# Optimization experiments

Measured on AMD Instinct MI355X. Metric: run time of the kernel, lower is better.

Reference implementation:

```python
import jax, jax.numpy as jnp
import numpy as np

N = 50000
E = 800000
IN, H, OUT = 128, 96, 64
BN_EPS = 1e-5


def setup_inputs() -> dict:
    key = jax.random.key(0)
    ks = jax.random.split(key, 16)
    x = jax.random.normal(ks[0], (N, IN), dtype=jnp.float32)
    edge_index = jax.random.randint(ks[1], (2, E), 0, N, dtype=jnp.int64)
    edge_weight = jax.random.uniform(ks[2], (E,), dtype=jnp.float32)
    def lin(k, fo, fi):
        # PyG glorot-ish init
        s = 1.0 / np.sqrt(fi)
        return jax.random.uniform(k, (fo, fi), minval=-s, maxval=s, dtype=jnp.float32)
    W1, b1 = lin(ks[3], H, IN), jnp.zeros((H,), jnp.float32)
    W2, b2 = lin(ks[4], H, H), jnp.zeros((H,), jnp.float32)
    W3, b3 = lin(ks[5], OUT, H), jnp.zeros((OUT,), jnp.float32)
    g1 = jnp.ones((H,), jnp.float32); beta1 = jnp.zeros((H,), jnp.float32)
    m1 = 0.1 * jax.random.normal(ks[6], (H,), dtype=jnp.float32)
    v1 = jnp.abs(1.0 + 0.1 * jax.random.normal(ks[7], (H,), dtype=jnp.float32))
    g2 = jnp.ones((H,), jnp.float32); beta2 = jnp.zeros((H,), jnp.float32)
    m2 = 0.1 * jax.random.normal(ks[8], (H,), dtype=jnp.float32)
    v2 = jnp.abs(1.0 + 0.1 * jax.random.normal(ks[9], (H,), dtype=jnp.float32))
    return dict(x=x, edge_index=edge_index, edge_weight=edge_weight,
                W1=W1, b1=b1, W2=W2, b2=b2, W3=W3, b3=b3,
                g1=g1, beta1=beta1, m1=m1, v1=v1,
                g2=g2, beta2=beta2, m2=m2, v2=v2)


def gcn_norm(edge_index, edge_weight, n):
    # PyG gcn_norm with add_self_loops=True, fill_value=1.0
    loop = jnp.arange(n, dtype=edge_index.dtype)
    row = jnp.concatenate([edge_index[0], loop])  # sources
    col = jnp.concatenate([edge_index[1], loop])  # targets
    ew = jnp.concatenate([edge_weight, jnp.ones((n,), edge_weight.dtype)])
    deg = jax.ops.segment_sum(ew, col, num_segments=n)
    dis = jnp.where(deg > 0, jax.lax.rsqrt(deg), 0.0)  # inf -> 0 masked_fill
    norm = dis[row] * ew * dis[col]
    return row, col, norm


def gcn_conv(x, row, col, norm, W, b, n):
    xw = x @ W.T                       # [N, F_out] dense transform first
    msg = norm[:, None] * xw[row]      # [E+N, F_out] gather + edge scale
    out = jax.ops.segment_sum(msg, col, num_segments=n)  # scatter-add
    return out + b


def bn_eval(x, gamma, beta, mean, var):
    return (x - mean) * jax.lax.rsqrt(var + BN_EPS) * gamma + beta


def reference(x, edge_index, edge_weight, W1, b1, W2, b2, W3, b3,
              g1, beta1, m1, v1, g2, beta2, m2, v2):
    n = x.shape[0]
    row, col, norm = gcn_norm(edge_index, edge_weight, n)  # cached=True: shared
    h = gcn_conv(x, row, col, norm, W1, b1, n)
    h = jax.nn.relu(bn_eval(h, g1, beta1, m1, v1))
    h = gcn_conv(h, row, col, norm, W2, b2, n)
    h = jax.nn.relu(bn_eval(h, g2, beta2, m2, v2))
    out = gcn_conv(h, row, col, norm, W3, b3, n)
    return out
```

## Files before the change

### kernel.cpp

```cpp
#include <hip/hip_runtime.h>
#include <hip/hip_fp16.h>


constexpr float BN_EPS = 1e-5f;
constexpr float DEG_SCALE = 131072.0f;
constexpr float INV_DEG_SCALE = 1.0f / 131072.0f;
constexpr float NORM_SCALE = 32768.0f;
constexpr float INV_NORM_SCALE = 1.0f / 32768.0f;

typedef _Float16 f16x8 __attribute__((ext_vector_type(8)));
typedef float f32x4 __attribute__((ext_vector_type(4)));


__device__ __forceinline__ void gemm1_q(const float* __restrict__ x,
                                        const float* __restrict__ W1,
                                        unsigned char* __restrict__ t1q,
                                        float* __restrict__ scl1,
                                        int n0b, int tid, int n,
                                        _Float16* lds, unsigned* rmaxb) {
    constexpr int LROW = 104;
    if (tid < 64) rmaxb[tid] = 0u;
    int wave = tid >> 6, lane = tid & 63, quad = lane >> 4, r = lane & 15;
    int n0 = n0b + wave * 16;
    if (n0 < n) {
        f16x8 a[4];
        const float* xr = x + (size_t)(n0 + r) * 128 + quad * 8;
#pragma unroll
        for (int kt = 0; kt < 4; ++kt) {
            float4 v0 = *(const float4*)(xr + kt * 32);
            float4 v1 = *(const float4*)(xr + kt * 32 + 4);
            f16x8 t = {(_Float16)v0.x, (_Float16)v0.y, (_Float16)v0.z, (_Float16)v0.w,
                       (_Float16)v1.x, (_Float16)v1.y, (_Float16)v1.z, (_Float16)v1.w};
            a[kt] = t;
        }
        f32x4 acc[6];
#pragma unroll
        for (int ft = 0; ft < 6; ++ft) acc[ft] = (f32x4){0.f, 0.f, 0.f, 0.f};
#pragma unroll
        for (int kt = 0; kt < 4; ++kt) {
#pragma unroll
            for (int ft = 0; ft < 6; ++ft) {
                const float* wr = W1 + (size_t)(ft * 16 + r) * 128 + kt * 32 + quad * 8;
                float4 v0 = *(const float4*)wr;
                float4 v1 = *(const float4*)(wr + 4);
                f16x8 b = {(_Float16)v0.x, (_Float16)v0.y, (_Float16)v0.z, (_Float16)v0.w,
                           (_Float16)v1.x, (_Float16)v1.y, (_Float16)v1.z, (_Float16)v1.w};
                acc[ft] = __builtin_amdgcn_mfma_f32_16x16x32_f16(a[kt], b, acc[ft], 0, 0, 0);
            }
        }
#pragma unroll
        for (int ft = 0; ft < 6; ++ft)
#pragma unroll
            for (int reg = 0; reg < 4; ++reg)
                lds[(size_t)(wave * 16 + quad * 4 + reg) * LROW + ft * 16 + r] =
                    (_Float16)acc[ft][reg];
    }
    __syncthreads();
    {
        int row = tid >> 2, qt = tid & 3;
        const _Float16* lp = lds + (size_t)row * LROW + qt * 24;
        float mx = 0.f;
#pragma unroll
        for (int j = 0; j < 24; ++j) mx = fmaxf(mx, fabsf((float)lp[j]));
        atomicMax(&rmaxb[row], __float_as_uint(mx));
    }
    __syncthreads();
    for (int i = tid; i < 64 * 12; i += 256) {
        int row = i / 12, c = i - row * 12;
        int grow = n0b + row;
        if (grow >= n) continue;
        float rm = __uint_as_float(rmaxb[row]);
        float inv = (rm > 0.f) ? 127.0f / rm : 0.f;
        const _Float16* lp = lds + (size_t)row * LROW + c * 8;
        unsigned lo = 0, hi = 0;
#pragma unroll
        for (int j = 0; j < 4; ++j) {
            int qv = __float2int_rn((float)lp[j] * inv);
            qv = qv > 127 ? 127 : (qv < -127 ? -127 : qv);
            lo |= ((unsigned)qv & 255u) << (8 * j);
        }
#pragma unroll
        for (int j = 0; j < 4; ++j) {
            int qv = __float2int_rn((float)lp[4 + j] * inv);
            qv = qv > 127 ? 127 : (qv < -127 ? -127 : qv);
            hi |= ((unsigned)qv & 255u) << (8 * j);
        }
        *(uint2*)(t1q + (size_t)grow * 96 + c * 8) = make_uint2(lo, hi);
        if (c == 0) scl1[grow] = rm * (1.0f / 127.0f);
    }
}

__global__ __launch_bounds__(256) void k_mega(
    const int* __restrict__ row_idx, const int* __restrict__ col_idx,
    const float* __restrict__ ew,
    unsigned long long* packed, unsigned char* rank, int e_cnt, int pair_b,
    int t1, int t2,
    const float* __restrict__ x, const float* __restrict__ W1,
    unsigned char* __restrict__ t1q, float* __restrict__ scl1, int n,
    const float* __restrict__ W2, const float* __restrict__ W3,
    _Float16* __restrict__ w2h, _Float16* __restrict__ w3h,
    int w2n4, int w3n4) {
    __shared__ _Float16 lds[64 * 104];
    __shared__ unsigned rmaxb[64];
    int b = blockIdx.x;
    if (b < 2 * pair_b) {
        int q = b >> 1;
        if ((b & 1) == 0) {
#pragma unroll
            for (int j = 0; j < 4; ++j) {
                int e = q * 1024 + j * 256 + (int)threadIdx.x;
                if (e < e_cnt) {
                    int c = col_idx[e];
                    int r = row_idx[e];
                    int t = (r >= t2) ? 2 : ((r >= t1) ? 1 : 0);
                    int sh = 24 + 10 * t;
                    unsigned wfix = (unsigned)(ew[e] * DEG_SCALE + 0.5f);
                    unsigned long long inc = (1ull << sh) | (unsigned long long)wfix;
                    unsigned long long old = atomicAdd(&packed[c], inc);
                    rank[e] = (unsigned char)((old >> sh) & 0x3FFull);
                }
            }
        } else {
            gemm1_q(x, W1, t1q, scl1, q * 64, (int)threadIdx.x, n, lds, rmaxb);
        }
    } else {
        int i = (b - 2 * pair_b) * 256 + (int)threadIdx.x;
        const float* src; _Float16* dst; int o;
        if (i < w2n4) { src = W2; dst = w2h; o = i; }
        else if (i < w2n4 + w3n4) { src = W3; dst = w3h; o = i - w2n4; }
        else return;
        float4 v = ((const float4*)src)[o];
        __half2 h0 = __floats2half2_rn(v.x, v.y);
        __half2 h1 = __floats2half2_rn(v.z, v.w);
        *(uint2*)(dst + (size_t)o * 4) = make_uint2(*(unsigned*)&h0, *(unsigned*)&h1);
    }
}


__device__ __forceinline__ int pk_cnt(unsigned long long p) {
    return (int)((p >> 24) & 0x3FF) + (int)((p >> 34) & 0x3FF) + (int)((p >> 44) & 0x3FF);
}

__global__ void k_scan1(const unsigned long long* __restrict__ packed,
                        int* bsum, float* dis, int n) {
    __shared__ int s[256];
    int i = blockIdx.x * 256 + threadIdx.x;
    int cnt = 0;
    if (i < n) {
        unsigned long long p = packed[i];
        cnt = pk_cnt(p);
        float wsum = (float)(unsigned)(p & 0xFFFFFFull) * INV_DEG_SCALE;
        dis[i] = rsqrtf(1.0f + wsum);
    }
    s[threadIdx.x] = cnt;
    __syncthreads();
    for (int off = 128; off > 0; off >>= 1) {
        if ((int)threadIdx.x < off) s[threadIdx.x] += s[threadIdx.x + off];
        __syncthreads();
    }
    if (threadIdx.x == 0) bsum[blockIdx.x] = s[0];
}

__global__ void k_scan23(const unsigned long long* __restrict__ packed,
                         const int* __restrict__ bsum,
                         int* row_ptr, int n, int e_total, int nb) {
    __shared__ int sb[256];
    __shared__ int s[256];
    int t = threadIdx.x;
    int bv = (t < nb) ? bsum[t] : 0;
    sb[t] = bv;
    __syncthreads();
    for (int off = 1; off < 256; off <<= 1) {
        int x = (t >= off) ? sb[t - off] : 0;
        __syncthreads();
        sb[t] += x;
        __syncthreads();
    }
    int boff = (blockIdx.x == 0) ? 0 : sb[blockIdx.x - 1];

    int i = blockIdx.x * 256 + t;
    int v = (i < n) ? pk_cnt(packed[i]) : 0;
    s[t] = v;
    __syncthreads();
    for (int off = 1; off < 256; off <<= 1) {
        int x = (t >= off) ? s[t - off] : 0;
        __syncthreads();
        s[t] += x;
        __syncthreads();
    }
    int ex = s[t] - v + boff;
    if (i < n) row_ptr[i] = ex;
    if (i == 0) row_ptr[n] = e_total;
}

__global__ void k_fill(const int* __restrict__ row_idx, const int* __restrict__ col_idx,
                       const float* __restrict__ ew, const float* __restrict__ dis,
                       const int* __restrict__ row_ptr, const unsigned char* __restrict__ rank,
                       const unsigned long long* __restrict__ packed,
                       unsigned* ep, int e_cnt, int t1, int t2) {
    int e = blockIdx.x * 256 + threadIdx.x;
    if (e < e_cnt) {
        int r = row_idx[e];
        int c = col_idx[e];
        unsigned long long p = packed[c];
        int c0 = (int)((p >> 24) & 0x3FF);
        int c1 = (int)((p >> 34) & 0x3FF);
        int t = (r >= t2) ? 2 : ((r >= t1) ? 1 : 0);
        int off = (t > 0 ? c0 : 0) + (t > 1 ? c1 : 0);
        float nm = dis[r] * ew[e];
        unsigned q = (unsigned)(nm * NORM_SCALE + 0.5f);
        if (q > 65535u) q = 65535u;
        ep[row_ptr[c] + off + (int)rank[e]] = ((unsigned)r << 16) | q;
    }
}


__device__ inline void cvt8(uint4 u, float* f) {
    float2 t;
    t = __half22float2(*(const __half2*)&u.x); f[0] = t.x; f[1] = t.y;
    t = __half22float2(*(const __half2*)&u.y); f[2] = t.x; f[3] = t.y;
    t = __half22float2(*(const __half2*)&u.z); f[4] = t.x; f[5] = t.y;
    t = __half22float2(*(const __half2*)&u.w); f[6] = t.x; f[7] = t.y;
}

__device__ inline void h8_acc(uint4 u, float w, float acc[8]) {
    float2 a = __half22float2(*(const __half2*)&u.x);
    float2 b = __half22float2(*(const __half2*)&u.y);
    float2 c = __half22float2(*(const __half2*)&u.z);
    float2 d = __half22float2(*(const __half2*)&u.w);
    acc[0] = fmaf(w, a.x, acc[0]); acc[1] = fmaf(w, a.y, acc[1]);
    acc[2] = fmaf(w, b.x, acc[2]); acc[3] = fmaf(w, b.y, acc[3]);
    acc[4] = fmaf(w, c.x, acc[4]); acc[5] = fmaf(w, c.y, acc[5]);
    acc[6] = fmaf(w, d.x, acc[6]); acc[7] = fmaf(w, d.y, acc[7]);
}

__device__ inline void q8_acc(uint2 v, float ws, float acc[8]) {
    int a = (int)v.x, b = (int)v.y;
    acc[0] = fmaf(ws, (float)(int)(char)(a      ), acc[0]);
    acc[1] = fmaf(ws, (float)(int)(char)(a >>  8), acc[1]);
    acc[2] = fmaf(ws, (float)(int)(char)(a >> 16), acc[2]);
    acc[3] = fmaf(ws, (float)(a >> 24),            acc[3]);
    acc[4] = fmaf(ws, (float)(int)(char)(b      ), acc[4]);
    acc[5] = fmaf(ws, (float)(int)(char)(b >>  8), acc[5]);
    acc[6] = fmaf(ws, (float)(int)(char)(b >> 16), acc[6]);
    acc[7] = fmaf(ws, (float)(b >> 24),            acc[7]);
}

__device__ __forceinline__ void gather_row_q(const unsigned char* __restrict__ tq,
                                             const float* __restrict__ scl,
                                             const unsigned* __restrict__ ep,
                                             int e0, int e1, int q, float acc[8]) {
    int e = e0;
    for (; e + 4 <= e1; e += 4) {
        unsigned p0 = ep[e + 0], p1 = ep[e + 1], p2 = ep[e + 2], p3 = ep[e + 3];
        uint2 v0 = *(const uint2*)(tq + (size_t)(p0 >> 16) * 96 + q * 8);
        uint2 v1 = *(const uint2*)(tq + (size_t)(p1 >> 16) * 96 + q * 8);
        uint2 v2 = *(const uint2*)(tq + (size_t)(p2 >> 16) * 96 + q * 8);
        uint2 v3 = *(const uint2*)(tq + (size_t)(p3 >> 16) * 96 + q * 8);
        float s0 = scl[p0 >> 16], s1 = scl[p1 >> 16];
        float s2 = scl[p2 >> 16], s3 = scl[p3 >> 16];
        q8_acc(v0, (float)(p0 & 0xffffu) * INV_NORM_SCALE * s0, acc);
        q8_acc(v1, (float)(p1 & 0xffffu) * INV_NORM_SCALE * s1, acc);
        q8_acc(v2, (float)(p2 & 0xffffu) * INV_NORM_SCALE * s2, acc);
        q8_acc(v3, (float)(p3 & 0xffffu) * INV_NORM_SCALE * s3, acc);
    }
    for (; e < e1; ++e) {
        unsigned p = ep[e];
        uint2 v = *(const uint2*)(tq + (size_t)(p >> 16) * 96 + q * 8);
        q8_acc(v, (float)(p & 0xffffu) * INV_NORM_SCALE * scl[p >> 16], acc);
    }
}

template <int FQ>
__device__ __forceinline__ void gather_row(const uint4* __restrict__ base,
                                           const unsigned* __restrict__ ep,
                                           int e0, int e1, int q, float acc[8]) {
    int e = e0;
    for (; e + 8 <= e1; e += 8) {
        unsigned p0 = ep[e + 0], p1 = ep[e + 1], p2 = ep[e + 2], p3 = ep[e + 3];
        unsigned p4 = ep[e + 4], p5 = ep[e + 5], p6 = ep[e + 6], p7 = ep[e + 7];
        uint4 x0 = base[(size_t)(p0 >> 16) * FQ + q];
        uint4 x1 = base[(size_t)(p1 >> 16) * FQ + q];
        uint4 x2 = base[(size_t)(p2 >> 16) * FQ + q];
        uint4 x3 = base[(size_t)(p3 >> 16) * FQ + q];
        uint4 x4 = base[(size_t)(p4 >> 16) * FQ + q];
        uint4 x5 = base[(size_t)(p5 >> 16) * FQ + q];
        uint4 x6 = base[(size_t)(p6 >> 16) * FQ + q];
        uint4 x7 = base[(size_t)(p7 >> 16) * FQ + q];
        h8_acc(x0, (float)(p0 & 0xffffu) * INV_NORM_SCALE, acc);
        h8_acc(x1, (float)(p1 & 0xffffu) * INV_NORM_SCALE, acc);
        h8_acc(x2, (float)(p2 & 0xffffu) * INV_NORM_SCALE, acc);
        h8_acc(x3, (float)(p3 & 0xffffu) * INV_NORM_SCALE, acc);
        h8_acc(x4, (float)(p4 & 0xffffu) * INV_NORM_SCALE, acc);
        h8_acc(x5, (float)(p5 & 0xffffu) * INV_NORM_SCALE, acc);
        h8_acc(x6, (float)(p6 & 0xffffu) * INV_NORM_SCALE, acc);
        h8_acc(x7, (float)(p7 & 0xffffu) * INV_NORM_SCALE, acc);
    }
    for (; e + 4 <= e1; e += 4) {
        unsigned p0 = ep[e + 0], p1 = ep[e + 1], p2 = ep[e + 2], p3 = ep[e + 3];
        uint4 x0 = base[(size_t)(p0 >> 16) * FQ + q];
        uint4 x1 = base[(size_t)(p1 >> 16) * FQ + q];
        uint4 x2 = base[(size_t)(p2 >> 16) * FQ + q];
        uint4 x3 = base[(size_t)(p3 >> 16) * FQ + q];
        h8_acc(x0, (float)(p0 & 0xffffu) * INV_NORM_SCALE, acc);
        h8_acc(x1, (float)(p1 & 0xffffu) * INV_NORM_SCALE, acc);
        h8_acc(x2, (float)(p2 & 0xffffu) * INV_NORM_SCALE, acc);
        h8_acc(x3, (float)(p3 & 0xffffu) * INV_NORM_SCALE, acc);
    }
    for (; e < e1; ++e) {
        unsigned p = ep[e];
        uint4 xv = base[(size_t)(p >> 16) * FQ + q];
        h8_acc(xv, (float)(p & 0xffffu) * INV_NORM_SCALE, acc);
    }
}


template <int FOUT, bool QOUT>
__global__ __launch_bounds__(192) void k_aggr_mm(
    const unsigned char* __restrict__ tq, const float* __restrict__ scl,
    const int* __restrict__ row_ptr, const unsigned* __restrict__ ep,
    const float* __restrict__ dis, const float* __restrict__ bias,
    const float* __restrict__ g, const float* __restrict__ beta,
    const float* __restrict__ m, const float* __restrict__ v,
    const _Float16* __restrict__ Wh,
    void* __restrict__ Yout, float* __restrict__ sclo, int n) {
    constexpr int LROW = 104;
    __shared__ _Float16 lds[16 * LROW];
    __shared__ unsigned rmaxb[16];
    int tid = (int)threadIdx.x;
    int n0b = blockIdx.x * 16;
    int nl = tid / 12;
    int q = tid - nl * 12;
    int node = n0b + nl;
    if (QOUT && tid < 16) rmaxb[tid] = 0u;

    if (node < n) {
        float d = dis[node];
        float acc[8];
#pragma unroll
        for (int j = 0; j < 8; ++j) acc[j] = 0.f;
        {
            uint2 sv = *(const uint2*)(tq + (size_t)node * 96 + q * 8);
            q8_acc(sv, d * scl[node], acc);
        }
        gather_row_q(tq, scl, ep, row_ptr[node], row_ptr[node + 1], q, acc);

        int fb = q * 8;
        const float4* bb = (const float4*)(bias + fb);
        float4 b0 = bb[0], b1 = bb[1];
        acc[0] = fmaf(acc[0], d, b0.x); acc[1] = fmaf(acc[1], d, b0.y);
        acc[2] = fmaf(acc[2], d, b0.z); acc[3] = fmaf(acc[3], d, b0.w);
        acc[4] = fmaf(acc[4], d, b1.x); acc[5] = fmaf(acc[5], d, b1.y);
        acc[6] = fmaf(acc[6], d, b1.z); acc[7] = fmaf(acc[7], d, b1.w);
#pragma unroll
        for (int j = 0; j < 8; ++j) {
            acc[j] = fmaxf((acc[j] - m[fb + j]) * rsqrtf(v[fb + j] + BN_EPS) * g[fb + j]
                           + beta[fb + j], 0.f);
        }
        __half2 h0 = __floats2half2_rn(acc[0], acc[1]);
        __half2 h1 = __floats2half2_rn(acc[2], acc[3]);
        __half2 h2 = __floats2half2_rn(acc[4], acc[5]);
        __half2 h3 = __floats2half2_rn(acc[6], acc[7]);
        *(uint4*)(lds + (size_t)nl * LROW + fb) =
            make_uint4(*(unsigned*)&h0, *(unsigned*)&h1, *(unsigned*)&h2, *(unsigned*)&h3);
    }
    __syncthreads();

    constexpr int FT = FOUT / 16;
    f32x4 cacc[FT];
    int quad = tid >> 4, r = tid & 15;
    if (tid < 64) {
        f16x8 a[3];
#pragma unroll
        for (int kt = 0; kt < 3; ++kt)
            a[kt] = *(const f16x8*)(lds + (size_t)r * LROW + kt * 32 + quad * 8);
#pragma unroll
        for (int ft = 0; ft < FT; ++ft) cacc[ft] = (f32x4){0.f, 0.f, 0.f, 0.f};
#pragma unroll
        for (int kt = 0; kt < 3; ++kt) {
#pragma unroll
            for (int ft = 0; ft < FT; ++ft) {
                f16x8 b = *(const f16x8*)(Wh + (size_t)(ft * 16 + r) * 96 + kt * 32 + quad * 8);
                cacc[ft] = __builtin_amdgcn_mfma_f32_16x16x32_f16(a[kt], b, cacc[ft], 0, 0, 0);
            }
        }
    }
    __syncthreads();
    if (tid < 64) {
#pragma unroll
        for (int ft = 0; ft < FT; ++ft)
#pragma unroll
            for (int reg = 0; reg < 4; ++reg)
                lds[(size_t)(quad * 4 + reg) * LROW + ft * 16 + r] = (_Float16)cacc[ft][reg];
    }
    __syncthreads();

    if (QOUT) {
        if (tid < 64) {
            int row = tid >> 2, qt = tid & 3;
            const _Float16* lp = lds + (size_t)row * LROW + qt * 24;
            float mx = 0.f;
#pragma unroll
            for (int j = 0; j < 24; ++j) mx = fmaxf(mx, fabsf((float)lp[j]));
            atomicMax(&rmaxb[row], __float_as_uint(mx));
        }
        __syncthreads();
        {
            int row = nl, c = q;
            int grow = n0b + row;
            if (grow < n) {
                float rm = __uint_as_float(rmaxb[row]);
                float inv = (rm > 0.f) ? 127.0f / rm : 0.f;
                const _Float16* lp = lds + (size_t)row * LROW + c * 8;
                unsigned lo = 0, hi = 0;
#pragma unroll
                for (int j = 0; j < 4; ++j) {
                    int qv = __float2int_rn((float)lp[j] * inv);
                    qv = qv > 127 ? 127 : (qv < -127 ? -127 : qv);
                    lo |= ((unsigned)qv & 255u) << (8 * j);
                }
#pragma unroll
                for (int j = 0; j < 4; ++j) {
                    int qv = __float2int_rn((float)lp[4 + j] * inv);
                    qv = qv > 127 ? 127 : (qv < -127 ? -127 : qv);
                    hi |= ((unsigned)qv & 255u) << (8 * j);
                }
                *(uint2*)((unsigned char*)Yout + (size_t)grow * 96 + c * 8) =
                    make_uint2(lo, hi);
                if (c == 0) sclo[grow] = rm * (1.0f / 127.0f);
            }
        }
    } else {
        constexpr int CPR = FOUT / 8;
        for (int i = tid; i < 16 * CPR; i += 192) {
            int row = i / CPR, c = i - row * CPR;
            int grow = n0b + row;
            if (grow < n)
                *(uint4*)((_Float16*)Yout + (size_t)grow * FOUT + c * 8) =
                    *(const uint4*)(lds + (size_t)row * LROW + c * 8);
        }
    }
}


__global__ __launch_bounds__(256) void k_aggr3(
    const _Float16* __restrict__ xw, const int* __restrict__ row_ptr,
    const unsigned* __restrict__ ep,
    const float* __restrict__ dis, const float* __restrict__ bias,
    float* __restrict__ out, int n) {
    constexpr int FQ = 8;
    int tg = blockIdx.x * 256 + threadIdx.x;
    int node = tg / FQ;
    int q = tg - node * FQ;
    if (node >= n) return;

    const uint4* __restrict__ base = (const uint4*)xw;
    float d = dis[node];
    float acc[8];
    {
        uint4 sv = base[(size_t)node * FQ + q];
        float t[8];
        cvt8(sv, t);
#pragma unroll
        for (int j = 0; j < 8; ++j) acc[j] = d * t[j];
    }
    gather_row<FQ>(base, ep, row_ptr[node], row_ptr[node + 1], q, acc);

    int fb = q * 8;
    const float4* bb = (const float4*)(bias + fb);
    float4 b0 = bb[0], b1 = bb[1];
    acc[0] = fmaf(acc[0], d, b0.x); acc[1] = fmaf(acc[1], d, b0.y);
    acc[2] = fmaf(acc[2], d, b0.z); acc[3] = fmaf(acc[3], d, b0.w);
    acc[4] = fmaf(acc[4], d, b1.x); acc[5] = fmaf(acc[5], d, b1.y);
    acc[6] = fmaf(acc[6], d, b1.z); acc[7] = fmaf(acc[7], d, b1.w);

    float* op = out + (size_t)node * 64 + fb;
    *(float4*)(op + 0) = make_float4(acc[0], acc[1], acc[2], acc[3]);
    *(float4*)(op + 4) = make_float4(acc[4], acc[5], acc[6], acc[7]);
}


extern "C" void kernel_launch(void* const* d_in, const int* in_sizes, int n_in,
                              void* d_out, int out_size, void* d_ws, size_t ws_size,
                              hipStream_t stream) {
    constexpr int IN = 128, H = 96, OUT = 64;

    const float* x   = (const float*)d_in[0];
    const int*   ei  = (const int*)d_in[1];
    const float* ew  = (const float*)d_in[2];
    const float* W1  = (const float*)d_in[3];
    const float* b1  = (const float*)d_in[4];
    const float* W2  = (const float*)d_in[5];
    const float* b2  = (const float*)d_in[6];
    const float* W3  = (const float*)d_in[7];
    const float* b3  = (const float*)d_in[8];
    const float* g1  = (const float*)d_in[9];
    const float* be1 = (const float*)d_in[10];
    const float* m1  = (const float*)d_in[11];
    const float* v1  = (const float*)d_in[12];
    const float* g2  = (const float*)d_in[13];
    const float* be2 = (const float*)d_in[14];
    const float* m2  = (const float*)d_in[15];
    const float* v2  = (const float*)d_in[16];

    const int N = in_sizes[0] / IN;
    const int E = in_sizes[2];
    const int* row_idx = ei;
    const int* col_idx = ei + E;
    const int T1 = N / 3, T2 = 2 * (N / 3);

    char* ws = (char*)d_ws;
    size_t off = 0;
    auto alloc = [&](size_t bytes) -> void* {
        void* p = ws + off;
        off = (off + bytes + 255) & ~(size_t)255;
        return p;
    };
    unsigned long long* packed = (unsigned long long*)alloc((size_t)N * 8);
    float*     dis     = (float*)alloc((size_t)N * 4);
    int*       row_ptr = (int*)alloc((size_t)(N + 1) * 4);
    int*       bsum    = (int*)alloc(256 * 4);
    unsigned char* rank = (unsigned char*)alloc((size_t)E);
    unsigned*  ep      = (unsigned*)alloc((size_t)E * 4);
    _Float16*  w2h     = (_Float16*)alloc((size_t)H * H * 2);
    _Float16*  w3h     = (_Float16*)alloc((size_t)OUT * H * 2);
    unsigned char* t1q = (unsigned char*)alloc((size_t)N * 96);
    float*     scl1    = (float*)alloc((size_t)N * 4);
    unsigned char* t2q = (unsigned char*)alloc((size_t)N * 96);
    float*     scl2    = (float*)alloc((size_t)N * 4);
    _Float16*  buf64   = (_Float16*)alloc((size_t)N * OUT * 2);
    (void)ws_size; (void)n_in; (void)out_size;

    constexpr int W2N4 = H * H / 4, W3N4 = OUT * H / 4;
    const int NB = (N + 255) / 256;
    const int DEG1024 = (E + 1023) / 1024;
    const int GG = (N + 63) / 64;
    const int PAIR = (DEG1024 > GG) ? DEG1024 : GG;
    const int CVT_B = (W2N4 + W3N4 + 255) / 256;

    hipMemsetAsync(packed, 0, (size_t)N * 8, stream);
    k_mega<<<2 * PAIR + CVT_B, 256, 0, stream>>>(
        row_idx, col_idx, ew, packed, rank, E, PAIR, T1, T2,
        x, W1, t1q, scl1, N, W2, W3, w2h, w3h, W2N4, W3N4);
    k_scan1<<<NB, 256, 0, stream>>>(packed, bsum, dis, N);
    k_scan23<<<NB, 256, 0, stream>>>(packed, bsum, row_ptr, N, E, NB);
    k_fill<<<(E + 255) / 256, 256, 0, stream>>>(row_idx, col_idx, ew, dis,
                                                row_ptr, rank, packed, ep, E, T1, T2);

    const int GF = (N + 15) / 16;
    const int GA64 = ((size_t)N * (OUT / 8) + 255) / 256;

    k_aggr_mm<H, true><<<GF, 192, 0, stream>>>(
        t1q, scl1, row_ptr, ep, dis, b1, g1, be1, m1, v1, w2h, t2q, scl2, N);

    k_aggr_mm<OUT, false><<<GF, 192, 0, stream>>>(
        t2q, scl2, row_ptr, ep, dis, b2, g2, be2, m2, v2, w3h, buf64, nullptr, N);

    k_aggr3<<<GA64, 256, 0, stream>>>(buf64, row_ptr, ep, dis, b3, (float*)d_out, N);
}
```

Measured before the change: 243.9 us.

## Replace global-atomic CSR build with two-level bucketed counting sort

Builds the destination-sorted edge list with a radix-style two-pass sort instead of per-edge 64-bit global atomics. Each chunk of edges builds a 256-bucket histogram in shared memory, a column scan produces per-chunk bucket bases, and a scatter writes edge records into coarse buckets. A per-bucket fine pass then counts and places edges by destination and source third using shared-memory atomics and computes degrees. A final pass rescales the edge norms by the source degree. This removes global atomic contention and the memset, but adds more kernel launches, an 8-byte intermediate record array, and a serial 768-entry prefix scan done by one thread per block.

```diff
diff --git a/kernel.cpp b/kernel.cpp
--- a/kernel.cpp
+++ b/kernel.cpp
@@ -3,8 +3,6 @@
 
 
 constexpr float BN_EPS = 1e-5f;
-constexpr float DEG_SCALE = 131072.0f;
-constexpr float INV_DEG_SCALE = 1.0f / 131072.0f;
 constexpr float NORM_SCALE = 32768.0f;
 constexpr float INV_NORM_SCALE = 1.0f / 32768.0f;
 
@@ -90,11 +88,12 @@
     }
 }
 
+
 __global__ __launch_bounds__(256) void k_mega(
-    const int* __restrict__ row_idx, const int* __restrict__ col_idx,
-    const float* __restrict__ ew,
-    unsigned long long* packed, unsigned char* rank, int e_cnt, int pair_b,
-    int t1, int t2,
+    const int* __restrict__ col_idx,
+    unsigned* __restrict__ H,
+    unsigned short* __restrict__ lrank,
+    int e_cnt, int pair_b,
     const float* __restrict__ x, const float* __restrict__ W1,
     unsigned char* __restrict__ t1q, float* __restrict__ scl1, int n,
     const float* __restrict__ W2, const float* __restrict__ W3,
@@ -102,24 +101,25 @@
     int w2n4, int w3n4) {
     __shared__ _Float16 lds[64 * 104];
     __shared__ unsigned rmaxb[64];
+    __shared__ unsigned hist[256];
     int b = blockIdx.x;
     if (b < 2 * pair_b) {
         int q = b >> 1;
         if ((b & 1) == 0) {
+            for (int t = threadIdx.x; t < 256; t += 256) hist[t] = 0;
+            __syncthreads();
 #pragma unroll
             for (int j = 0; j < 4; ++j) {
                 int e = q * 1024 + j * 256 + (int)threadIdx.x;
                 if (e < e_cnt) {
-                    int c = col_idx[e];
-                    int r = row_idx[e];
-                    int t = (r >= t2) ? 2 : ((r >= t1) ? 1 : 0);
-                    int sh = 24 + 10 * t;
-                    unsigned wfix = (unsigned)(ew[e] * DEG_SCALE + 0.5f);
-                    unsigned long long inc = (1ull << sh) | (unsigned long long)wfix;
-                    unsigned long long old = atomicAdd(&packed[c], inc);
-                    rank[e] = (unsigned char)((old >> sh) & 0x3FFull);
+                    int bk = col_idx[e] >> 8;
+                    unsigned lr = atomicAdd(&hist[bk], 1u);
+                    lrank[e] = (unsigned short)lr;
                 }
             }
+            __syncthreads();
+            for (int t = threadIdx.x; t < 256; t += 256)
+                H[(size_t)q * 256 + t] = hist[t];
         } else {
             gemm1_q(x, W1, t1q, scl1, q * 64, (int)threadIdx.x, n, lds, rmaxb);
         }
@@ -137,80 +137,137 @@
 }
 
 
-__device__ __forceinline__ int pk_cnt(unsigned long long p) {
-    return (int)((p >> 24) & 0x3FF) + (int)((p >> 34) & 0x3FF) + (int)((p >> 44) & 0x3FF);
-}
-
-__global__ void k_scan1(const unsigned long long* __restrict__ packed,
-                        int* bsum, float* dis, int n) {
-    __shared__ int s[256];
-    int i = blockIdx.x * 256 + threadIdx.x;
-    int cnt = 0;
-    if (i < n) {
-        unsigned long long p = packed[i];
-        cnt = pk_cnt(p);
-        float wsum = (float)(unsigned)(p & 0xFFFFFFull) * INV_DEG_SCALE;
-        dis[i] = rsqrtf(1.0f + wsum);
-    }
-    s[threadIdx.x] = cnt;
-    __syncthreads();
-    for (int off = 128; off > 0; off >>= 1) {
-        if ((int)threadIdx.x < off) s[threadIdx.x] += s[threadIdx.x + off];
+__global__ __launch_bounds__(256) void k_colscan(const unsigned* __restrict__ H,
+                                                 unsigned* __restrict__ Base,
+                                                 unsigned* __restrict__ total,
+                                                 int nblk) {
+    __shared__ unsigned s[256];
+    int bin = blockIdx.x;
+    int t = (int)threadIdx.x;
+    unsigned carry = 0;
+    int nch = (nblk + 255) / 256;
+    for (int c = 0; c < nch; ++c) {
+        int i = c * 256 + t;
+        unsigned v = (i < nblk) ? H[(size_t)i * 256 + bin] : 0;
         __syncthreads();
-    }
-    if (threadIdx.x == 0) bsum[blockIdx.x] = s[0];
-}
-
-__global__ void k_scan23(const unsigned long long* __restrict__ packed,
-                         const int* __restrict__ bsum,
-                         int* row_ptr, int n, int e_total, int nb) {
-    __shared__ int sb[256];
-    __shared__ int s[256];
-    int t = threadIdx.x;
-    int bv = (t < nb) ? bsum[t] : 0;
-    sb[t] = bv;
+        s[t] = v;
+        __syncthreads();
+        for (int off = 1; off < 256; off <<= 1) {
+            unsigned x = (t >= off) ? s[t - off] : 0;
+            __syncthreads();
+            s[t] += x;
+            __syncthreads();
+        }
+        if (i < nblk) Base[(size_t)i * 256 + bin] = carry + s[t] - v;
+        carry += s[255];
+    }
+    if (t == 0) total[bin] = carry;
+}
+
+
+__global__ void k_binoff(const unsigned* __restrict__ total,
+                         unsigned* __restrict__ boff, int nb, int e_total) {
+    __shared__ unsigned s[256];
+    int t = (int)threadIdx.x;
+    unsigned v = (t < nb) ? total[t] : 0;
+    s[t] = v;
     __syncthreads();
     for (int off = 1; off < 256; off <<= 1) {
-        int x = (t >= off) ? sb[t - off] : 0;
-        __syncthreads();
-        sb[t] += x;
-        __syncthreads();
-    }
-    int boff = (blockIdx.x == 0) ? 0 : sb[blockIdx.x - 1];
-
-    int i = blockIdx.x * 256 + t;
-    int v = (i < n) ? pk_cnt(packed[i]) : 0;
-    s[t] = v;
-    __syncthreads();
-    for (int off = 1; off < 256; off <<= 1) {
-        int x = (t >= off) ? s[t - off] : 0;
+        unsigned x = (t >= off) ? s[t - off] : 0;
         __syncthreads();
         s[t] += x;
         __syncthreads();
     }
-    int ex = s[t] - v + boff;
-    if (i < n) row_ptr[i] = ex;
-    if (i == 0) row_ptr[n] = e_total;
-}
-
-__global__ void k_fill(const int* __restrict__ row_idx, const int* __restrict__ col_idx,
-                       const float* __restrict__ ew, const float* __restrict__ dis,
-                       const int* __restrict__ row_ptr, const unsigned char* __restrict__ rank,
-                       const unsigned long long* __restrict__ packed,
-                       unsigned* ep, int e_cnt, int t1, int t2) {
+    if (t < nb) boff[t] = s[t] - v;
+    if (t == 0) boff[nb] = (unsigned)e_total;
+}
+
+
+__global__ __launch_bounds__(256) void k_scatter(
+    const int* __restrict__ row_idx, const int* __restrict__ col_idx,
+    const float* __restrict__ ew, const unsigned short* __restrict__ lrank,
+    const unsigned* __restrict__ Base, const unsigned* __restrict__ boff,
+    unsigned long long* __restrict__ recs, int e_cnt, int nbk) {
+    __shared__ unsigned base[256];
+    int q = blockIdx.x;
+    for (int t = threadIdx.x; t < 256; t += 256)
+        base[t] = (t < nbk) ? (boff[t] + Base[(size_t)q * 256 + t]) : 0u;
+    __syncthreads();
+#pragma unroll
+    for (int j = 0; j < 4; ++j) {
+        int e = q * 1024 + j * 256 + (int)threadIdx.x;
+        if (e < e_cnt) {
+            int c = col_idx[e];
+            int r = row_idx[e];
+            unsigned wfix = (unsigned)(ew[e] * NORM_SCALE + 0.5f);
+            if (wfix > 65535u) wfix = 65535u;
+            unsigned slot = base[c >> 8] + (unsigned)lrank[e];
+            recs[slot] = ((unsigned long long)(unsigned)(c & 255) << 32)
+                       | (unsigned long long)(((unsigned)r << 16) | wfix);
+        }
+    }
+}
+
+
+__global__ __launch_bounds__(256) void k_fine(
+    const unsigned long long* __restrict__ recs, const unsigned* __restrict__ boff,
+    int* __restrict__ row_ptr, float* __restrict__ dis,
+    unsigned* __restrict__ ep, int n, int t1, int t2) {
+    __shared__ unsigned cnt[768];
+    __shared__ unsigned ws[256];
+    int b = blockIdx.x;
+    int tid = (int)threadIdx.x;
+    unsigned e0 = boff[b], e1 = boff[b + 1];
+    for (int i = tid; i < 768; i += 256) cnt[i] = 0;
+    ws[tid] = 0;
+    __syncthreads();
+    for (unsigned e = e0 + (unsigned)tid; e < e1; e += 256) {
+        unsigned long long rec = recs[e];
+        int dlow = (int)((rec >> 32) & 255ull);
+        unsigned lo = (unsigned)rec;
+        int src = (int)(lo >> 16);
+        unsigned wfix = lo & 0xFFFFu;
+        int th = (src >= t2) ? 2 : (src >= t1) ? 1 : 0;
+        atomicAdd(&cnt[dlow * 3 + th], 1u);
+        atomicAdd(&ws[dlow], wfix);
+    }
+    __syncthreads();
+    if (tid == 0) {
+        unsigned run = 0;
+        for (int i = 0; i < 768; ++i) { unsigned v = cnt[i]; cnt[i] = run; run += v; }
+    }
+    __syncthreads();
+    {
+        int dest = b * 256 + tid;
+        if (dest < n) {
+            row_ptr[dest] = (int)(e0 + cnt[tid * 3]);
+            dis[dest] = rsqrtf(1.0f + (float)ws[tid] * INV_NORM_SCALE);
+        }
+        if (b == (int)gridDim.x - 1 && tid == 0) row_ptr[n] = (int)e1;
+    }
+    __syncthreads();
+    for (unsigned e = e0 + (unsigned)tid; e < e1; e += 256) {
+        unsigned long long rec = recs[e];
+        int dlow = (int)((rec >> 32) & 255ull);
+        unsigned lo = (unsigned)rec;
+        int src = (int)(lo >> 16);
+        int th = (src >= t2) ? 2 : (src >= t1) ? 1 : 0;
+        unsigned slot = e0 + atomicAdd(&cnt[dlow * 3 + th], 1u);
+        ep[slot] = lo;
+    }
+}
+
+
+__global__ void k_fill2(unsigned* __restrict__ ep, const float* __restrict__ dis,
+                        int e_cnt) {
     int e = blockIdx.x * 256 + threadIdx.x;
     if (e < e_cnt) {
-        int r = row_idx[e];
-        int c = col_idx[e];
-        unsigned long long p = packed[c];
-        int c0 = (int)((p >> 24) & 0x3FF);
-        int c1 = (int)((p >> 34) & 0x3FF);
-        int t = (r >= t2) ? 2 : ((r >= t1) ? 1 : 0);
-        int off = (t > 0 ? c0 : 0) + (t > 1 ? c1 : 0);
-        float nm = dis[r] * ew[e];
-        unsigned q = (unsigned)(nm * NORM_SCALE + 0.5f);
-        if (q > 65535u) q = 65535u;
-        ep[row_ptr[c] + off + (int)rank[e]] = ((unsigned)r << 16) | q;
+        unsigned v = ep[e];
+        int src = (int)(v >> 16);
+        float qf = dis[src] * (float)(v & 0xFFFFu);
+        unsigned qi = (unsigned)(qf + 0.5f);
+        if (qi > 65535u) qi = 65535u;
+        ep[e] = (v & 0xFFFF0000u) | qi;
     }
 }
 
@@ -508,6 +565,8 @@
     const int* row_idx = ei;
     const int* col_idx = ei + E;
     const int T1 = N / 3, T2 = 2 * (N / 3);
+    const int NBUCK = (N + 255) / 256;
+    const int DEG1024 = (E + 1023) / 1024;
 
     char* ws = (char*)d_ws;
     size_t off = 0;
@@ -516,11 +575,14 @@
         off = (off + bytes + 255) & ~(size_t)255;
         return p;
     };
-    unsigned long long* packed = (unsigned long long*)alloc((size_t)N * 8);
+    unsigned*  Hc      = (unsigned*)alloc((size_t)DEG1024 * 256 * 4);
+    unsigned*  Basec   = (unsigned*)alloc((size_t)DEG1024 * 256 * 4);
+    unsigned*  total   = (unsigned*)alloc(256 * 4);
+    unsigned*  boff    = (unsigned*)alloc(257 * 4);
+    unsigned short* lrank = (unsigned short*)alloc((size_t)E * 2);
+    unsigned long long* recs = (unsigned long long*)alloc((size_t)E * 8);
+    int*       row_ptr = (int*)alloc((size_t)(N + 1) * 4);
     float*     dis     = (float*)alloc((size_t)N * 4);
-    int*       row_ptr = (int*)alloc((size_t)(N + 1) * 4);
-    int*       bsum    = (int*)alloc(256 * 4);
-    unsigned char* rank = (unsigned char*)alloc((size_t)E);
     unsigned*  ep      = (unsigned*)alloc((size_t)E * 4);
     _Float16*  w2h     = (_Float16*)alloc((size_t)H * H * 2);
     _Float16*  w3h     = (_Float16*)alloc((size_t)OUT * H * 2);
@@ -532,20 +594,19 @@
     (void)ws_size; (void)n_in; (void)out_size;
 
     constexpr int W2N4 = H * H / 4, W3N4 = OUT * H / 4;
-    const int NB = (N + 255) / 256;
-    const int DEG1024 = (E + 1023) / 1024;
     const int GG = (N + 63) / 64;
     const int PAIR = (DEG1024 > GG) ? DEG1024 : GG;
     const int CVT_B = (W2N4 + W3N4 + 255) / 256;
 
-    hipMemsetAsync(packed, 0, (size_t)N * 8, stream);
     k_mega<<<2 * PAIR + CVT_B, 256, 0, stream>>>(
-        row_idx, col_idx, ew, packed, rank, E, PAIR, T1, T2,
+        col_idx, Hc, lrank, E, PAIR,
         x, W1, t1q, scl1, N, W2, W3, w2h, w3h, W2N4, W3N4);
-    k_scan1<<<NB, 256, 0, stream>>>(packed, bsum, dis, N);
-    k_scan23<<<NB, 256, 0, stream>>>(packed, bsum, row_ptr, N, E, NB);
-    k_fill<<<(E + 255) / 256, 256, 0, stream>>>(row_idx, col_idx, ew, dis,
-                                                row_ptr, rank, packed, ep, E, T1, T2);
+    k_colscan<<<NBUCK, 256, 0, stream>>>(Hc, Basec, total, DEG1024);
+    k_binoff<<<1, 256, 0, stream>>>(total, boff, NBUCK, E);
+    k_scatter<<<DEG1024, 256, 0, stream>>>(row_idx, col_idx, ew, lrank,
+                                           Basec, boff, recs, E, NBUCK);
+    k_fine<<<NBUCK, 256, 0, stream>>>(recs, boff, row_ptr, dis, ep, N, T1, T2);
+    k_fill2<<<(E + 255) / 256, 256, 0, stream>>>(ep, dis, E);
 
     const int GF = (N + 15) / 16;
     const int GA64 = ((size_t)N * (OUT / 8) + 255) / 256;
```

After: 264.0 us. +8.2%, slower.
